# Optimization experiments

Measured on AMD Instinct MI355X. Metric: run time of the kernel, lower is better.

Reference implementation:

```python
import jax, jax.numpy as jnp
import numpy as np

N = 100000
E = 1600000
D_IN = 128
D_H = 128


def _glorot(key, shape):
    fan_in, fan_out = shape[1], shape[0]
    lim = np.sqrt(6.0 / (fan_in + fan_out))
    return jax.random.uniform(key, shape, jnp.float32, -lim, lim)


def setup_inputs() -> dict:
    key = jax.random.key(0)
    ks = jax.random.split(key, 12)
    x = jax.random.normal(ks[0], (N, D_IN), jnp.float32)
    edge_index = jax.random.randint(ks[1], (2, E), 0, N, jnp.int64)
    return {
        "x": x,
        "edge_index": edge_index,
        # lin1, lin2 (nn.Linear: y = x @ W.T + b)
        "W1": _glorot(ks[2], (D_H, D_IN)),
        "b1": jnp.zeros((D_H,), jnp.float32),
        "W2": _glorot(ks[3], (D_H, D_H)),
        "b2": jnp.zeros((D_H,), jnp.float32),
        # SAGEConv1: lin_l (neighbors, with bias), lin_r (root, no bias)
        "c1_Wl": _glorot(ks[4], (D_H, D_H)),
        "c1_bl": jnp.zeros((D_H,), jnp.float32),
        "c1_Wr": _glorot(ks[5], (D_H, D_H)),
        # SAGEConv2
        "c2_Wl": _glorot(ks[6], (D_H, D_H)),
        "c2_bl": jnp.zeros((D_H,), jnp.float32),
        "c2_Wr": _glorot(ks[7], (D_H, D_H)),
    }


def _sage_conv(h, src, dst, Wl, bl, Wr, num_nodes):
    # PyG SAGEConv (mean aggr): out = lin_l(mean_{j in N(i)} h_j) + lin_r(h_i)
    msgs = h[src]  # [E, D] gather
    agg = jax.ops.segment_sum(msgs, dst, num_segments=num_nodes)  # [N, D]
    deg = jax.ops.segment_sum(jnp.ones((src.shape[0],), h.dtype), dst,
                              num_segments=num_nodes)
    mean = agg / jnp.maximum(deg, 1.0)[:, None]
    return mean @ Wl.T + bl + h @ Wr.T


def reference(x, edge_index, W1, b1, W2, b2,
              c1_Wl, c1_bl, c1_Wr, c2_Wl, c2_bl, c2_Wr):
    src, dst = edge_index[0], edge_index[1]
    n = x.shape[0]
    h = jax.nn.relu(x @ W1.T + b1)
    h = jax.nn.relu(_sage_conv(h, src, dst, c1_Wl, c1_bl, c1_Wr, n))
    h = jax.nn.relu(h @ W2.T + b2)
    h = jax.nn.relu(_sage_conv(h, src, dst, c2_Wl, c2_bl, c2_Wr, n))
    return h
```

## Files before the change

kernel.cpp:

```cpp
#include <hip/hip_runtime.h>
#include <hip/hip_bf16.h>

#define NN 100000
#define EE 1600000
#define DD 128

#define BSH 9
#define NBUK ((NN + 511) / 512)
#define EPB 8192

typedef __attribute__((ext_vector_type(8))) _Float16 half8;
typedef __attribute__((ext_vector_type(2))) _Float16 half2v;
typedef __attribute__((ext_vector_type(4))) float f32x4;

__global__ void k_detect(const long long* __restrict__ ei64, int* __restrict__ flag) {
    __shared__ int ok;
    if (threadIdx.x == 0) ok = 1;
    __syncthreads();
    long long v = ei64[threadIdx.x];
    if (v < 0 || v >= (long long)NN) atomicAnd(&ok, 0);
    __syncthreads();
    if (threadIdx.x == 0) *flag = ok;
}

__device__ inline int load_edge(const int* ei32, const long long* ei64, int is64, size_t pos) {
    return is64 ? (int)ei64[pos] : ei32[pos];
}

__global__ __launch_bounds__(1024) void k_bhist(const int* __restrict__ ei32,
                                                const long long* __restrict__ ei64,
                                                const int* __restrict__ flag,
                                                int* __restrict__ bcnt) {
    __shared__ int h[NBUK];
    int t = threadIdx.x;
    if (t < NBUK) h[t] = 0;
    __syncthreads();
    int is64 = *flag;
    int base = blockIdx.x * EPB;
    int end = min(base + EPB, EE);
    for (int e = base + t; e < end; e += 1024) {
        int d = load_edge(ei32, ei64, is64, (size_t)EE + e);
        atomicAdd(&h[d >> BSH], 1);
    }
    __syncthreads();
    if (t < NBUK && h[t] > 0) atomicAdd(&bcnt[t], h[t]);
}

__global__ __launch_bounds__(256) void k_bscan(const int* __restrict__ bcnt,
                                               int* __restrict__ bbase,
                                               int* __restrict__ bcur) {
    __shared__ int sm[256];
    int t = threadIdx.x;
    int v = (t < NBUK) ? bcnt[t] : 0;
    sm[t] = v;
    __syncthreads();
    for (int off = 1; off < 256; off <<= 1) {
        int u = (t >= off) ? sm[t - off] : 0;
        __syncthreads();
        sm[t] += u;
        __syncthreads();
    }
    if (t < NBUK) {
        int b = sm[t] - v;
        bbase[t] = b;
        bcur[t] = b;
    }
    if (t == 0) bbase[NBUK] = EE;
}

__global__ __launch_bounds__(1024) void k_part(const int* __restrict__ ei32,
                                               const long long* __restrict__ ei64,
                                               const int* __restrict__ flag,
                                               int* __restrict__ bcur,
                                               unsigned* __restrict__ eb) {
    __shared__ int h[NBUK];
    __shared__ int cbase[NBUK];
    int t = threadIdx.x;
    if (t < NBUK) h[t] = 0;
    __syncthreads();
    int is64 = *flag;
    int base = blockIdx.x * EPB;
    int end = min(base + EPB, EE);
    int mys[8], myd[8];
    int cnt_i = 0;
    for (int e = base + t; e < end; e += 1024) {
        int s = load_edge(ei32, ei64, is64, (size_t)e);
        int d = load_edge(ei32, ei64, is64, (size_t)EE + e);
        mys[cnt_i] = s;
        myd[cnt_i] = d;
        ++cnt_i;
        atomicAdd(&h[d >> BSH], 1);
    }
    __syncthreads();
    if (t < NBUK && h[t] > 0) cbase[t] = atomicAdd(&bcur[t], h[t]);
    __syncthreads();
    if (t < NBUK) h[t] = 0;
    __syncthreads();
    for (int i = 0; i < cnt_i; ++i) {
        int b = myd[i] >> BSH;
        int slot = atomicAdd(&h[b], 1);
        unsigned v = (unsigned)mys[i] | ((unsigned)(myd[i] & 511) << 17);
        eb[cbase[b] + slot] = v;
    }
}

__global__ __launch_bounds__(1024) void k_bucket(const unsigned* __restrict__ eb,
                                                 const int* __restrict__ bbase,
                                                 int* __restrict__ rp,
                                                 int* __restrict__ ssrc) {
    __shared__ int ncnt[512];
    __shared__ int cur[512];
    int b = blockIdx.x, t = threadIdx.x;
    int ebeg = bbase[b], eend = bbase[b + 1];
    int nodeBase = b << BSH;
    int nNodes = min(512, NN - nodeBase);
    if (t < 512) ncnt[t] = 0;
    __syncthreads();
    for (int i = ebeg + t; i < eend; i += 1024) {
        unsigned v = eb[i];
        atomicAdd(&ncnt[v >> 17], 1);
    }
    __syncthreads();
    int own = (t < 512) ? ncnt[t] : 0;
    for (int off = 1; off < 512; off <<= 1) {
        int u = (t >= off && t < 512) ? ncnt[t - off] : 0;
        __syncthreads();
        if (t < 512) ncnt[t] += u;
        __syncthreads();
    }
    if (t < 512) {
        int excl = ncnt[t] - own;
        cur[t] = ebeg + excl;
        if (t < nNodes) rp[nodeBase + t] = ebeg + excl;
    }
    __syncthreads();
    for (int i = ebeg + t; i < eend; i += 1024) {
        unsigned v = eb[i];
        int slot = atomicAdd(&cur[v >> 17], 1);
        ssrc[slot] = (int)(v & 0x1FFFFu);
    }
    if (b == 0 && t == 0) rp[NN] = EE;
}

__global__ void k_prepw(const float* __restrict__ w0, const float* __restrict__ w1,
                        const float* __restrict__ w2, const float* __restrict__ w3,
                        const float* __restrict__ w4, const float* __restrict__ w5,
                        _Float16* __restrict__ whi) {
    int i = blockIdx.x * 256 + threadIdx.x;
    if (i >= 6 * 16384) return;
    int slot = i >> 14, idx = i & 16383;
    const float* w = slot == 0 ? w0 : slot == 1 ? w1 : slot == 2 ? w2
                   : slot == 3 ? w3 : slot == 4 ? w4 : w5;
    whi[i] = (_Float16)w[idx];
}

#define WSTR 136

template <bool DUAL, bool AF16, bool OF16>
__global__ __launch_bounds__(256) void k_gemm(const void* __restrict__ A,
                                              const _Float16* __restrict__ W1g,
                                              const void* __restrict__ A2,
                                              const _Float16* __restrict__ W2g,
                                              const float* __restrict__ bias,
                                              void* __restrict__ out) {
    __shared__ _Float16 sW[128 * WSTR];
    int t = threadIdx.x;
    int wave = t >> 6;
    int lane = t & 63;
    int lr = lane & 15;
    int lk = lane >> 4;
    int rowBase = blockIdx.x * 128 + wave * 32;

    f32x4 acc[2][8];
#pragma unroll
    for (int mt = 0; mt < 2; ++mt)
#pragma unroll
        for (int nt = 0; nt < 8; ++nt) acc[mt][nt] = (f32x4){0.f, 0.f, 0.f, 0.f};

    const int NPASS = DUAL ? 2 : 1;
    for (int pass = 0; pass < NPASS; ++pass) {
        const _Float16* Wg = pass ? W2g : W1g;
        const void* Ap = pass ? A2 : A;
        if (pass) __syncthreads();
#pragma unroll
        for (int i = 0; i < 8; ++i) {
            int c = t + i * 256;
            int n = c >> 4, j = c & 15;
            *(half8*)(sW + n * WSTR + j * 8) = *(const half8*)(Wg + n * 128 + j * 8);
        }
        __syncthreads();

#pragma unroll
        for (int ks = 0; ks < 4; ++ks) {
            int kf = ks * 32 + lk * 8;
            half8 b[8];
#pragma unroll
            for (int nt = 0; nt < 8; ++nt)
                b[nt] = *(const half8*)(sW + (nt * 16 + lr) * WSTR + (ks * 4 + lk) * 8);
#pragma unroll
            for (int mt = 0; mt < 2; ++mt) {
                int row = rowBase + mt * 16 + lr;
                int rc = row < NN ? row : NN - 1;
                if (AF16) {
                    half8 a = *(const half8*)((const _Float16*)Ap + (size_t)rc * 128 + kf);
#pragma unroll
                    for (int nt = 0; nt < 8; ++nt)
                        acc[mt][nt] = __builtin_amdgcn_mfma_f32_16x16x32_f16(a, b[nt], acc[mt][nt], 0, 0, 0);
                } else {
                    const float* ap = (const float*)Ap + (size_t)rc * 128 + kf;
                    float4 a0 = *(const float4*)ap;
                    float4 a1 = *(const float4*)(ap + 4);
                    float av[8] = {a0.x, a0.y, a0.z, a0.w, a1.x, a1.y, a1.z, a1.w};
                    half8 ah, al;
#pragma unroll
                    for (int j = 0; j < 8; ++j) {
                        _Float16 h = (_Float16)av[j];
                        ah[j] = h;
                        al[j] = (_Float16)(av[j] - (float)h);
                    }
#pragma unroll
                    for (int nt = 0; nt < 8; ++nt) {
                        acc[mt][nt] = __builtin_amdgcn_mfma_f32_16x16x32_f16(ah, b[nt], acc[mt][nt], 0, 0, 0);
                        acc[mt][nt] = __builtin_amdgcn_mfma_f32_16x16x32_f16(al, b[nt], acc[mt][nt], 0, 0, 0);
                    }
                }
            }
        }
    }

#pragma unroll
    for (int mt = 0; mt < 2; ++mt) {
#pragma unroll
        for (int nt = 0; nt < 8; ++nt) {
            int col = nt * 16 + lr;
            float b = bias[col];
#pragma unroll
            for (int r = 0; r < 4; ++r) {
                int row = rowBase + mt * 16 + lk * 4 + r;
                if (row < NN) {
                    float v = acc[mt][nt][r] + b;
                    v = v > 0.f ? v : 0.f;
                    if (OF16)
                        ((_Float16*)out)[(size_t)row * 128 + col] = (_Float16)v;
                    else
                        ((float*)out)[(size_t)row * 128 + col] = v;
                }
            }
        }
    }
}

__global__ __launch_bounds__(256) void k_agg(const _Float16* __restrict__ h,
                                             const int* __restrict__ rp,
                                             const int* __restrict__ ssrc,
                                             _Float16* __restrict__ out) {
    int wid = (int)((blockIdx.x * 256 + threadIdx.x) >> 6);
    int lane = threadIdx.x & 63;
    if (wid >= NN) return;
    int g = lane >> 4;
    int f = lane & 15;
    int s = __builtin_amdgcn_readfirstlane(rp[wid]);
    int e = __builtin_amdgcn_readfirstlane(rp[wid + 1]);
    int deg = e - s;

    float acc[8] = {0.f, 0.f, 0.f, 0.f, 0.f, 0.f, 0.f, 0.f};
    for (int j = s; j < e; j += 16) {
        int j0 = j + g, j1 = j + 4 + g, j2 = j + 8 + g, j3 = j + 12 + g;
        int r0 = ssrc[j0 < e ? j0 : s];
        int r1 = ssrc[j1 < e ? j1 : s];
        int r2 = ssrc[j2 < e ? j2 : s];
        int r3 = ssrc[j3 < e ? j3 : s];
        half8 v0 = *(const half8*)(h + (size_t)r0 * 128 + f * 8);
        half8 v1 = *(const half8*)(h + (size_t)r1 * 128 + f * 8);
        half8 v2 = *(const half8*)(h + (size_t)r2 * 128 + f * 8);
        half8 v3 = *(const half8*)(h + (size_t)r3 * 128 + f * 8);
        float m0 = j0 < e ? 1.f : 0.f;
        float m1 = j1 < e ? 1.f : 0.f;
        float m2 = j2 < e ? 1.f : 0.f;
        float m3 = j3 < e ? 1.f : 0.f;
#pragma unroll
        for (int q = 0; q < 8; ++q) {
            acc[q] += m0 * (float)v0[q] + m1 * (float)v1[q]
                    + m2 * (float)v2[q] + m3 * (float)v3[q];
        }
    }
#pragma unroll
    for (int q = 0; q < 8; ++q) {
        acc[q] += __shfl_xor(acc[q], 16, 64);
        acc[q] += __shfl_xor(acc[q], 32, 64);
    }
    float inv = deg > 0 ? 1.0f / (float)deg : 0.f;
    if (g == 0) {
        half8 o;
#pragma unroll
        for (int q = 0; q < 8; ++q) o[q] = (_Float16)(acc[q] * inv);
        *(half8*)(out + (size_t)wid * 128 + f * 8) = o;
    }
}

extern "C" void kernel_launch(void* const* d_in, const int* in_sizes, int n_in,
                              void* d_out, int out_size, void* d_ws, size_t ws_size,
                              hipStream_t stream) {
    const float* x = (const float*)d_in[0];
    const int* ei32 = (const int*)d_in[1];
    const long long* ei64 = (const long long*)d_in[1];
    const float* b1 = (const float*)d_in[3];
    const float* b2 = (const float*)d_in[5];
    const float* c1_bl = (const float*)d_in[7];
    const float* c2_bl = (const float*)d_in[10];

    char* ws = (char*)d_ws;
    const size_t H16 = (size_t)NN * 128 * 2;
    _Float16* hH = (_Float16*)ws;
    _Float16* aggH = (_Float16*)(ws + H16);
    int* ssrc = (int*)(ws + 2 * H16);
    int* rp = (int*)(ws + 2 * H16 + 6400000);
    int* bufs = (int*)(ws + 2 * H16 + 6400000 + 400128);
    _Float16* whi = (_Float16*)(ws + 2 * H16 + 6400000 + 2 * 400128);
    int* flag = (int*)((char*)(whi + 6 * 16384));

    int* bcnt = bufs;
    int* bbase = bufs + 256;
    int* bcur = bufs + 512;
    unsigned* eb = (unsigned*)hH;

    k_detect<<<1, 256, 0, stream>>>(ei64, flag);
    hipMemsetAsync(bcnt, 0, NBUK * 4, stream);
    int pgrid = (EE + EPB - 1) / EPB;
    k_bhist<<<pgrid, 1024, 0, stream>>>(ei32, ei64, flag, bcnt);
    k_bscan<<<1, 256, 0, stream>>>(bcnt, bbase, bcur);
    k_part<<<pgrid, 1024, 0, stream>>>(ei32, ei64, flag, bcur, eb);
    k_bucket<<<NBUK, 1024, 0, stream>>>(eb, bbase, rp, ssrc);
    k_prepw<<<(6 * 16384 + 255) / 256, 256, 0, stream>>>(
        (const float*)d_in[2], (const float*)d_in[6], (const float*)d_in[8],
        (const float*)d_in[4], (const float*)d_in[9], (const float*)d_in[11], whi);

    dim3 g((NN + 127) / 128);
    int agrid = (NN + 3) / 4;
    k_gemm<false, false, true><<<g, 256, 0, stream>>>(
        x, whi + 0 * 16384, nullptr, nullptr, b1, hH);
    k_agg<<<agrid, 256, 0, stream>>>(hH, rp, ssrc, aggH);
    k_gemm<true, true, true><<<g, 256, 0, stream>>>(
        aggH, whi + 1 * 16384, hH, whi + 2 * 16384, c1_bl, aggH);
    k_gemm<false, true, true><<<g, 256, 0, stream>>>(
        aggH, whi + 3 * 16384, nullptr, nullptr, b2, hH);
    k_agg<<<agrid, 256, 0, stream>>>(hH, rp, ssrc, aggH);
    k_gemm<true, true, false><<<g, 256, 0, stream>>>(
        aggH, whi + 4 * 16384, hH, whi + 5 * 16384, c2_bl, d_out);
}
```

Baseline: 391.3 us.

## Fold edge-format detection and weight conversion into consumers, drop atomics and memset

Removes the standalone detect kernel, the memset and the weight-conversion kernel. Each partition block now checks the index dtype with a wave vote, and each GEMM block converts fp32 weights to fp16 while staging them into shared memory. The bucket histogram is written per block and reduced in the scan kernel instead of using global atomics. The partition kernel re-reads edges rather than holding them in registers. The aggregation kernel now sums pairs of fp16 values in half precision before converting to fp32, and skips masking on full 16-edge chunks. Costs: extra global reads of the edges and weights, and slightly lower accumulation precision.

```diff
diff --git a/kernel.cpp b/kernel.cpp
--- a/kernel.cpp
+++ b/kernel.cpp
@@ -8,19 +8,16 @@
 #define BSH 9
 #define NBUK ((NN + 511) / 512)
 #define EPB 8192
+#define PGRID ((EE + EPB - 1) / EPB)
 
 typedef __attribute__((ext_vector_type(8))) _Float16 half8;
+typedef __attribute__((ext_vector_type(4))) _Float16 half4;
 typedef __attribute__((ext_vector_type(2))) _Float16 half2v;
 typedef __attribute__((ext_vector_type(4))) float f32x4;
 
-__global__ void k_detect(const long long* __restrict__ ei64, int* __restrict__ flag) {
-    __shared__ int ok;
-    if (threadIdx.x == 0) ok = 1;
-    __syncthreads();
-    long long v = ei64[threadIdx.x];
-    if (v < 0 || v >= (long long)NN) atomicAnd(&ok, 0);
-    __syncthreads();
-    if (threadIdx.x == 0) *flag = ok;
+__device__ inline int detect64(const long long* __restrict__ ei64) {
+    long long v = ei64[threadIdx.x & 63];
+    return __all(v >= 0 && v < (long long)NN);
 }
 
 __device__ inline int load_edge(const int* ei32, const long long* ei64, int is64, size_t pos) {
@@ -29,13 +26,12 @@
 
 __global__ __launch_bounds__(1024) void k_bhist(const int* __restrict__ ei32,
                                                 const long long* __restrict__ ei64,
-                                                const int* __restrict__ flag,
-                                                int* __restrict__ bcnt) {
+                                                int* __restrict__ bh) {
     __shared__ int h[NBUK];
     int t = threadIdx.x;
+    int is64 = detect64(ei64);
     if (t < NBUK) h[t] = 0;
     __syncthreads();
-    int is64 = *flag;
     int base = blockIdx.x * EPB;
     int end = min(base + EPB, EE);
     for (int e = base + t; e < end; e += 1024) {
@@ -43,15 +39,17 @@
         atomicAdd(&h[d >> BSH], 1);
     }
     __syncthreads();
-    if (t < NBUK && h[t] > 0) atomicAdd(&bcnt[t], h[t]);
-}
-
-__global__ __launch_bounds__(256) void k_bscan(const int* __restrict__ bcnt,
+    if (t < NBUK) bh[blockIdx.x * 256 + t] = h[t];
+}
+
+__global__ __launch_bounds__(256) void k_bscan(const int* __restrict__ bh,
                                                int* __restrict__ bbase,
                                                int* __restrict__ bcur) {
     __shared__ int sm[256];
     int t = threadIdx.x;
-    int v = (t < NBUK) ? bcnt[t] : 0;
+    int v = 0;
+    if (t < NBUK)
+        for (int b = 0; b < PGRID; ++b) v += bh[b * 256 + t];
     sm[t] = v;
     __syncthreads();
     for (int off = 1; off < 256; off <<= 1) {
@@ -70,37 +68,31 @@
 
 __global__ __launch_bounds__(1024) void k_part(const int* __restrict__ ei32,
                                                const long long* __restrict__ ei64,
-                                               const int* __restrict__ flag,
                                                int* __restrict__ bcur,
                                                unsigned* __restrict__ eb) {
     __shared__ int h[NBUK];
     __shared__ int cbase[NBUK];
     int t = threadIdx.x;
+    int is64 = detect64(ei64);
     if (t < NBUK) h[t] = 0;
     __syncthreads();
-    int is64 = *flag;
     int base = blockIdx.x * EPB;
     int end = min(base + EPB, EE);
-    int mys[8], myd[8];
-    int cnt_i = 0;
+    for (int e = base + t; e < end; e += 1024) {
+        int d = load_edge(ei32, ei64, is64, (size_t)EE + e);
+        atomicAdd(&h[d >> BSH], 1);
+    }
+    __syncthreads();
+    if (t < NBUK && h[t] > 0) cbase[t] = atomicAdd(&bcur[t], h[t]);
+    __syncthreads();
+    if (t < NBUK) h[t] = 0;
+    __syncthreads();
     for (int e = base + t; e < end; e += 1024) {
         int s = load_edge(ei32, ei64, is64, (size_t)e);
         int d = load_edge(ei32, ei64, is64, (size_t)EE + e);
-        mys[cnt_i] = s;
-        myd[cnt_i] = d;
-        ++cnt_i;
-        atomicAdd(&h[d >> BSH], 1);
-    }
-    __syncthreads();
-    if (t < NBUK && h[t] > 0) cbase[t] = atomicAdd(&bcur[t], h[t]);
-    __syncthreads();
-    if (t < NBUK) h[t] = 0;
-    __syncthreads();
-    for (int i = 0; i < cnt_i; ++i) {
-        int b = myd[i] >> BSH;
+        int b = d >> BSH;
         int slot = atomicAdd(&h[b], 1);
-        unsigned v = (unsigned)mys[i] | ((unsigned)(myd[i] & 511) << 17);
-        eb[cbase[b] + slot] = v;
+        eb[cbase[b] + slot] = (unsigned)s | ((unsigned)(d & 511) << 17);
     }
 }
 
@@ -142,25 +134,26 @@
     if (b == 0 && t == 0) rp[NN] = EE;
 }
 
-__global__ void k_prepw(const float* __restrict__ w0, const float* __restrict__ w1,
-                        const float* __restrict__ w2, const float* __restrict__ w3,
-                        const float* __restrict__ w4, const float* __restrict__ w5,
-                        _Float16* __restrict__ whi) {
-    int i = blockIdx.x * 256 + threadIdx.x;
-    if (i >= 6 * 16384) return;
-    int slot = i >> 14, idx = i & 16383;
-    const float* w = slot == 0 ? w0 : slot == 1 ? w1 : slot == 2 ? w2
-                   : slot == 3 ? w3 : slot == 4 ? w4 : w5;
-    whi[i] = (_Float16)w[idx];
-}
-
 #define WSTR 136
+
+__device__ inline void stageW(const float* __restrict__ Wg, _Float16* sW, int t) {
+#pragma unroll
+    for (int i = 0; i < 16; ++i) {
+        int c = t + i * 256;
+        int n = c >> 5, j = c & 31;
+        float4 w = ((const float4*)Wg)[c];
+        half4 o;
+        o[0] = (_Float16)w.x; o[1] = (_Float16)w.y;
+        o[2] = (_Float16)w.z; o[3] = (_Float16)w.w;
+        *(half4*)(sW + n * WSTR + j * 4) = o;
+    }
+}
 
 template <bool DUAL, bool AF16, bool OF16>
 __global__ __launch_bounds__(256) void k_gemm(const void* __restrict__ A,
-                                              const _Float16* __restrict__ W1g,
+                                              const float* __restrict__ W1g,
                                               const void* __restrict__ A2,
-                                              const _Float16* __restrict__ W2g,
+                                              const float* __restrict__ W2g,
                                               const float* __restrict__ bias,
                                               void* __restrict__ out) {
     __shared__ _Float16 sW[128 * WSTR];
@@ -179,15 +172,10 @@
 
     const int NPASS = DUAL ? 2 : 1;
     for (int pass = 0; pass < NPASS; ++pass) {
-        const _Float16* Wg = pass ? W2g : W1g;
+        const float* Wg = pass ? W2g : W1g;
         const void* Ap = pass ? A2 : A;
         if (pass) __syncthreads();
-#pragma unroll
-        for (int i = 0; i < 8; ++i) {
-            int c = t + i * 256;
-            int n = c >> 4, j = c & 15;
-            *(half8*)(sW + n * WSTR + j * 8) = *(const half8*)(Wg + n * 128 + j * 8);
-        }
+        stageW(Wg, sW, t);
         __syncthreads();
 
 #pragma unroll
@@ -196,7 +184,7 @@
             half8 b[8];
 #pragma unroll
             for (int nt = 0; nt < 8; ++nt)
-                b[nt] = *(const half8*)(sW + (nt * 16 + lr) * WSTR + (ks * 4 + lk) * 8);
+                b[nt] = *(const half8*)(sW + (nt * 16 + lr) * WSTR + kf);
 #pragma unroll
             for (int mt = 0; mt < 2; ++mt) {
                 int row = rowBase + mt * 16 + lr;
@@ -263,7 +251,10 @@
     int e = __builtin_amdgcn_readfirstlane(rp[wid + 1]);
     int deg = e - s;
 
-    float acc[8] = {0.f, 0.f, 0.f, 0.f, 0.f, 0.f, 0.f, 0.f};
+    const half2v ONE = {(_Float16)1.f, (_Float16)1.f};
+    const half2v ZER = {(_Float16)0.f, (_Float16)0.f};
+    float fa[8] = {0.f, 0.f, 0.f, 0.f, 0.f, 0.f, 0.f, 0.f};
+
     for (int j = s; j < e; j += 16) {
         int j0 = j + g, j1 = j + 4 + g, j2 = j + 8 + g, j3 = j + 12 + g;
         int r0 = ssrc[j0 < e ? j0 : s];
@@ -274,26 +265,46 @@
         half8 v1 = *(const half8*)(h + (size_t)r1 * 128 + f * 8);
         half8 v2 = *(const half8*)(h + (size_t)r2 * 128 + f * 8);
         half8 v3 = *(const half8*)(h + (size_t)r3 * 128 + f * 8);
-        float m0 = j0 < e ? 1.f : 0.f;
-        float m1 = j1 < e ? 1.f : 0.f;
-        float m2 = j2 < e ? 1.f : 0.f;
-        float m3 = j3 < e ? 1.f : 0.f;
-#pragma unroll
-        for (int q = 0; q < 8; ++q) {
-            acc[q] += m0 * (float)v0[q] + m1 * (float)v1[q]
-                    + m2 * (float)v2[q] + m3 * (float)v3[q];
+        if (j + 16 <= e) {
+#pragma unroll
+            for (int q = 0; q < 4; ++q) {
+                half2v p0 = {v0[2 * q], v0[2 * q + 1]};
+                half2v p1 = {v1[2 * q], v1[2 * q + 1]};
+                half2v p2 = {v2[2 * q], v2[2 * q + 1]};
+                half2v p3 = {v3[2 * q], v3[2 * q + 1]};
+                half2v sA = p0 + p1;
+                half2v sB = p2 + p3;
+                fa[2 * q]     += (float)sA.x + (float)sB.x;
+                fa[2 * q + 1] += (float)sA.y + (float)sB.y;
+            }
+        } else {
+            half2v m0 = j0 < e ? ONE : ZER;
+            half2v m1 = j1 < e ? ONE : ZER;
+            half2v m2 = j2 < e ? ONE : ZER;
+            half2v m3 = j3 < e ? ONE : ZER;
+#pragma unroll
+            for (int q = 0; q < 4; ++q) {
+                half2v p0 = {v0[2 * q], v0[2 * q + 1]};
+                half2v p1 = {v1[2 * q], v1[2 * q + 1]};
+                half2v p2 = {v2[2 * q], v2[2 * q + 1]};
+                half2v p3 = {v3[2 * q], v3[2 * q + 1]};
+                half2v sA = p0 * m0 + p1 * m1;
+                half2v sB = p2 * m2 + p3 * m3;
+                fa[2 * q]     += (float)sA.x + (float)sB.x;
+                fa[2 * q + 1] += (float)sA.y + (float)sB.y;
+            }
         }
     }
 #pragma unroll
     for (int q = 0; q < 8; ++q) {
-        acc[q] += __shfl_xor(acc[q], 16, 64);
-        acc[q] += __shfl_xor(acc[q], 32, 64);
+        fa[q] += __shfl_xor(fa[q], 16, 64);
+        fa[q] += __shfl_xor(fa[q], 32, 64);
     }
     float inv = deg > 0 ? 1.0f / (float)deg : 0.f;
     if (g == 0) {
         half8 o;
 #pragma unroll
-        for (int q = 0; q < 8; ++q) o[q] = (_Float16)(acc[q] * inv);
+        for (int q = 0; q < 8; ++q) o[q] = (_Float16)(fa[q] * inv);
         *(half8*)(out + (size_t)wid * 128 + f * 8) = o;
     }
 }
@@ -304,10 +315,16 @@
     const float* x = (const float*)d_in[0];
     const int* ei32 = (const int*)d_in[1];
     const long long* ei64 = (const long long*)d_in[1];
+    const float* W1 = (const float*)d_in[2];
     const float* b1 = (const float*)d_in[3];
+    const float* W2 = (const float*)d_in[4];
     const float* b2 = (const float*)d_in[5];
+    const float* c1Wl = (const float*)d_in[6];
     const float* c1_bl = (const float*)d_in[7];
+    const float* c1Wr = (const float*)d_in[8];
+    const float* c2Wl = (const float*)d_in[9];
     const float* c2_bl = (const float*)d_in[10];
+    const float* c2Wr = (const float*)d_in[11];
 
     char* ws = (char*)d_ws;
     const size_t H16 = (size_t)NN * 128 * 2;
@@ -315,36 +332,22 @@
     _Float16* aggH = (_Float16*)(ws + H16);
     int* ssrc = (int*)(ws + 2 * H16);
     int* rp = (int*)(ws + 2 * H16 + 6400000);
-    int* bufs = (int*)(ws + 2 * H16 + 6400000 + 400128);
-    _Float16* whi = (_Float16*)(ws + 2 * H16 + 6400000 + 2 * 400128);
-    int* flag = (int*)((char*)(whi + 6 * 16384));
-
-    int* bcnt = bufs;
-    int* bbase = bufs + 256;
-    int* bcur = bufs + 512;
+    int* bh = (int*)(ws + 2 * H16 + 6400000 + 400128);
+    int* bbase = bh + PGRID * 256;
+    int* bcur = bbase + 256;
     unsigned* eb = (unsigned*)hH;
 
-    k_detect<<<1, 256, 0, stream>>>(ei64, flag);
-    hipMemsetAsync(bcnt, 0, NBUK * 4, stream);
-    int pgrid = (EE + EPB - 1) / EPB;
-    k_bhist<<<pgrid, 1024, 0, stream>>>(ei32, ei64, flag, bcnt);
-    k_bscan<<<1, 256, 0, stream>>>(bcnt, bbase, bcur);
-    k_part<<<pgrid, 1024, 0, stream>>>(ei32, ei64, flag, bcur, eb);
+    k_bhist<<<PGRID, 1024, 0, stream>>>(ei32, ei64, bh);
+    k_bscan<<<1, 256, 0, stream>>>(bh, bbase, bcur);
+    k_part<<<PGRID, 1024, 0, stream>>>(ei32, ei64, bcur, eb);
     k_bucket<<<NBUK, 1024, 0, stream>>>(eb, bbase, rp, ssrc);
-    k_prepw<<<(6 * 16384 + 255) / 256, 256, 0, stream>>>(
-        (const float*)d_in[2], (const float*)d_in[6], (const float*)d_in[8],
-        (const float*)d_in[4], (const float*)d_in[9], (const float*)d_in[11], whi);
 
     dim3 g((NN + 127) / 128);
     int agrid = (NN + 3) / 4;
-    k_gemm<false, false, true><<<g, 256, 0, stream>>>(
-        x, whi + 0 * 16384, nullptr, nullptr, b1, hH);
+    k_gemm<false, false, true><<<g, 256, 0, stream>>>(x, W1, nullptr, nullptr, b1, hH);
     k_agg<<<agrid, 256, 0, stream>>>(hH, rp, ssrc, aggH);
-    k_gemm<true, true, true><<<g, 256, 0, stream>>>(
-        aggH, whi + 1 * 16384, hH, whi + 2 * 16384, c1_bl, aggH);
-    k_gemm<false, true, true><<<g, 256, 0, stream>>>(
-        aggH, whi + 3 * 16384, nullptr, nullptr, b2, hH);
+    k_gemm<true, true, true><<<g, 256, 0, stream>>>(aggH, c1Wl, hH, c1Wr, c1_bl, aggH);
+    k_gemm<false, true, true><<<g, 256, 0, stream>>>(aggH, W2, nullptr, nullptr, b2, hH);
     k_agg<<<agrid, 256, 0, stream>>>(hH, rp, ssrc, aggH);
-    k_gemm<true, true, false><<<g, 256, 0, stream>>>(
-        aggH, whi + 4 * 16384, hH, whi + 5 * 16384, c2_bl, d_out);
-}
+    k_gemm<true, true, false><<<g, 256, 0, stream>>>(aggH, c2Wl, hH, c2Wr, c2_bl, d_out);
+}
```

Result: slower. 420.5 us (+7.5%).
